# Optimization experiments

Measured on AMD Instinct MI355X. Metric: run time of the kernel, lower is better.

Reference implementation:

```python
import jax, jax.numpy as jnp
import numpy as np

SEQ_LEN, INPUT_DIM, HIDDEN_DIM, OUTPUT_DIM = 1024, 128, 256, 128
BATCH = 256


def setup_inputs() -> dict:
    key = jax.random.key(0)
    ks = jax.random.split(key, 12)
    s_x = 1.0 / np.sqrt(INPUT_DIM)
    s_h = 1.0 / np.sqrt(HIDDEN_DIM)
    def lin(k, fan_in, shape, scale):
        return jax.random.uniform(k, shape, jnp.float32, -scale, scale)
    inp = {"x": jax.random.normal(ks[0], (BATCH, SEQ_LEN, INPUT_DIM), jnp.float32)}
    names = ["g", "i", "f", "o"]
    for j, n in enumerate(names):
        inp[f"W{n}x"] = lin(ks[1 + 2 * j], INPUT_DIM, (HIDDEN_DIM, INPUT_DIM), s_x)
        inp[f"b{n}x"] = lin(jax.random.fold_in(ks[1 + 2 * j], 1), INPUT_DIM, (HIDDEN_DIM,), s_x)
        inp[f"W{n}h"] = lin(ks[2 + 2 * j], HIDDEN_DIM, (HIDDEN_DIM, HIDDEN_DIM), s_h)
    inp["Wp"] = lin(ks[9], HIDDEN_DIM, (OUTPUT_DIM, HIDDEN_DIM), s_h)
    inp["bp"] = lin(ks[10], HIDDEN_DIM, (OUTPUT_DIM,), s_h)
    return inp


def reference(x, Wgx, bgx, Wgh, Wix, bix, Wih, Wfx, bfx, Wfh, Wox, box, Woh, Wp, bp):
    B = x.shape[0]
    H = Wgh.shape[0]
    # Precompute all input projections in one batched GEMM per gate: (B,T,H)
    gx = jnp.einsum('bti,hi->bth', x, Wgx) + bgx
    ix = jnp.einsum('bti,hi->bth', x, Wix) + bix
    fx = jnp.einsum('bti,hi->bth', x, Wfx) + bfx
    ox = jnp.einsum('bti,hi->bth', x, Wox) + box
    xs = jnp.stack([gx, ix, fx, ox], axis=0).transpose(2, 0, 1, 3)  # (T,4,B,H)

    def step(carry, x_t):
        h, c = carry
        gx_t, ix_t, fx_t, ox_t = x_t[0], x_t[1], x_t[2], x_t[3]
        g = jnp.tanh(gx_t + h @ Wgh.T)
        i = jax.nn.sigmoid(ix_t + h @ Wih.T)
        f = jax.nn.sigmoid(fx_t + h @ Wfh.T)
        o = jax.nn.sigmoid(ox_t + h @ Woh.T)
        c = g * i + c * f
        h = jnp.tanh(c) * o
        return (h, c), None

    h0 = jnp.zeros((B, H), x.dtype)
    c0 = jnp.zeros((B, H), x.dtype)
    (h_T, _), _ = jax.lax.scan(step, (h0, c0), xs)
    return h_T @ Wp.T + bp
```

## Files before the change

### kernel.cpp

```cpp
#include <hip/hip_runtime.h>
#include <hip/hip_fp16.h>

#define TSEQ 1024
#define NBATCH 256
#define HD 256
#define ID 128
#define ODIM 128

typedef _Float16 f16;
typedef _Float16 f16x8 __attribute__((ext_vector_type(8)));
typedef float f32x4 __attribute__((ext_vector_type(4)));

__global__ void pack_weights(
    const float* __restrict__ Wgh, const float* __restrict__ Wih,
    const float* __restrict__ Wfh, const float* __restrict__ Woh,
    const float* __restrict__ Wgx, const float* __restrict__ Wix,
    const float* __restrict__ Wfx, const float* __restrict__ Wox,
    const float* __restrict__ bgx, const float* __restrict__ bix,
    const float* __restrict__ bfx, const float* __restrict__ box,
    f16* __restrict__ Whcat, f16* __restrict__ Wxcat, float* __restrict__ bcat)
{
    const int np = blockIdx.x;
    const int g  = (np >> 6) & 3;
    const int j  = np >> 8;
    const int uu = np & 63;
    const int u  = j * 64 + uu;
    const float* Wh = (g == 0) ? Wgh : (g == 1) ? Wih : (g == 2) ? Wfh : Woh;
    const float* Wx = (g == 0) ? Wgx : (g == 1) ? Wix : (g == 2) ? Wfx : Wox;
    const float* bx = (g == 0) ? bgx : (g == 1) ? bix : (g == 2) ? bfx : box;
    const int k = threadIdx.x;
    Whcat[np * 256 + k] = (f16)Wh[u * 256 + k];
    if (k < ID) Wxcat[np * ID + k] = (f16)Wx[u * ID + k];
    if (k == 0) bcat[np] = bx[u];
}

__global__ __launch_bounds__(256, 1) void lstm_rec(
    const float* __restrict__ x,
    const f16* __restrict__ Whcat,
    const f16* __restrict__ Wxcat,
    const float* __restrict__ bcat,
    f16* __restrict__ hbuf,
    float* __restrict__ hT,
    int* __restrict__ flags)
{
    const int tid  = threadIdx.x;
    const int lane = tid & 63;
    const int w    = tid >> 6;
    const int q    = lane >> 4;
    const int n    = lane & 15;
    const int bid  = blockIdx.x;
    const int grp  = bid >> 2;
    const int j    = bid & 3;
    const int b0   = grp * 16;

    f16x8 wh[4][8];
    f16x8 wx[4][4];
    float bias[4];
#pragma unroll
    for (int g = 0; g < 4; ++g) {
        const int row = j * 256 + g * 64 + w * 16 + n;
        bias[g] = bcat[row];
#pragma unroll
        for (int kk = 0; kk < 8; ++kk)
            wh[g][kk] = *(const f16x8*)&Whcat[row * 256 + kk * 32 + q * 8];
#pragma unroll
        for (int k4 = 0; k4 < 4; ++k4)
            wx[g][k4] = *(const f16x8*)&Wxcat[row * ID + k4 * 32 + q * 8];
    }

    float c[4] = {0.f, 0.f, 0.f, 0.f};
    const int uglob    = j * 64 + w * 16 + n;
    const int myslot   = (grp * 16 + j * 4 + w) * 64;
    const int pollslot = (grp * 16 + tid) * 64;

    const float* xrow = &x[(size_t)(b0 + n) * TSEQ * ID];
    float4 xr[8];
#pragma unroll
    for (int k4 = 0; k4 < 4; ++k4) {
        xr[k4 * 2]     = *(const float4*)&xrow[k4 * 32 + q * 8];
        xr[k4 * 2 + 1] = *(const float4*)&xrow[k4 * 32 + q * 8 + 4];
    }

    for (int t = 0; t < TSEQ; ++t) {
        f16x8 xa[4];
#pragma unroll
        for (int k4 = 0; k4 < 4; ++k4) {
            const float* f0 = (const float*)&xr[k4 * 2];
            const float* f1 = (const float*)&xr[k4 * 2 + 1];
#pragma unroll
            for (int e = 0; e < 4; ++e) {
                xa[k4][e]     = (f16)f0[e];
                xa[k4][4 + e] = (f16)f1[e];
            }
        }
        if (t + 1 < TSEQ) {
            const float* xp = &xrow[(size_t)(t + 1) * ID];
#pragma unroll
            for (int k4 = 0; k4 < 4; ++k4) {
                xr[k4 * 2]     = *(const float4*)&xp[k4 * 32 + q * 8];
                xr[k4 * 2 + 1] = *(const float4*)&xp[k4 * 32 + q * 8 + 4];
            }
        }

        f32x4 acc[4];
#pragma unroll
        for (int g = 0; g < 4; ++g) {
            f32x4 av = {bias[g], bias[g], bias[g], bias[g]};
            acc[g] = av;
        }
#pragma unroll
        for (int k4 = 0; k4 < 4; ++k4)
#pragma unroll
            for (int g = 0; g < 4; ++g)
                acc[g] = __builtin_amdgcn_mfma_f32_16x16x32_f16(xa[k4], wx[g][k4], acc[g], 0, 0, 0);

        if (t > 0) {
            if (tid < 16) {
                while (__hip_atomic_load(&flags[pollslot], __ATOMIC_RELAXED,
                                         __HIP_MEMORY_SCOPE_AGENT) < t)
                    __builtin_amdgcn_s_sleep(1);
            }
            __syncthreads();
            const unsigned long long* hp = (const unsigned long long*)
                &hbuf[(size_t)(((t - 1) & 1) * NBATCH + b0 + n) * HD];
            f16x8 ha[8];
#pragma unroll
            for (int kk = 0; kk < 8; ++kk) {
                union { unsigned long long u[2]; f16x8 v; } hu;
                hu.u[0] = __hip_atomic_load(hp + kk * 8 + q * 2,     __ATOMIC_RELAXED,
                                            __HIP_MEMORY_SCOPE_AGENT);
                hu.u[1] = __hip_atomic_load(hp + kk * 8 + q * 2 + 1, __ATOMIC_RELAXED,
                                            __HIP_MEMORY_SCOPE_AGENT);
                ha[kk] = hu.v;
            }
#pragma unroll
            for (int kk = 0; kk < 8; ++kk)
#pragma unroll
                for (int g = 0; g < 4; ++g)
                    acc[g] = __builtin_amdgcn_mfma_f32_16x16x32_f16(ha[kk], wh[g][kk], acc[g], 0, 0, 0);
        }

#pragma unroll
        for (int r = 0; r < 4; ++r) {
            const float gp_ = acc[0][r], ip_ = acc[1][r], fp_ = acc[2][r], op_ = acc[3][r];
            const float gg = 1.f - 2.f / (1.f + __expf(2.f * gp_));
            const float ii = 1.f / (1.f + __expf(-ip_));
            const float ff = 1.f / (1.f + __expf(-fp_));
            const float oo = 1.f / (1.f + __expf(-op_));
            c[r] = gg * ii + c[r] * ff;
            const float hh = (1.f - 2.f / (1.f + __expf(2.f * c[r]))) * oo;
            const int b = b0 + q * 4 + r;
            if (t < TSEQ - 1) {
                union { _Float16 f; unsigned short s; } cv;
                cv.f = (_Float16)hh;
                __hip_atomic_store((unsigned short*)&hbuf[(size_t)((t & 1) * NBATCH + b) * HD + uglob],
                                   cv.s, __ATOMIC_RELAXED, __HIP_MEMORY_SCOPE_AGENT);
            } else {
                hT[(size_t)b * HD + uglob] = hh;
            }
        }

        if (t < TSEQ - 1) {
            __atomic_signal_fence(__ATOMIC_SEQ_CST);
            __builtin_amdgcn_s_waitcnt(0x0F70);
            __atomic_signal_fence(__ATOMIC_SEQ_CST);
            if (lane == 0)
                __hip_atomic_store(&flags[myslot], t + 1, __ATOMIC_RELAXED,
                                   __HIP_MEMORY_SCOPE_AGENT);
        }
    }
}

__global__ void out_proj(const float* __restrict__ hT, const float* __restrict__ Wp,
                         const float* __restrict__ bp, float* __restrict__ out)
{
    const int b = blockIdx.x;
    const int o = threadIdx.x;
    __shared__ float hrow[HD];
    for (int u = threadIdx.x; u < HD; u += ODIM) hrow[u] = hT[b * HD + u];
    __syncthreads();
    float s = bp[o];
    const float* wr = &Wp[o * HD];
#pragma unroll 8
    for (int u = 0; u < HD; ++u) s += hrow[u] * wr[u];
    out[b * ODIM + o] = s;
}

extern "C" void kernel_launch(void* const* d_in, const int* in_sizes, int n_in,
                              void* d_out, int out_size, void* d_ws, size_t ws_size,
                              hipStream_t stream) {
    const float* x   = (const float*)d_in[0];
    const float* Wgx = (const float*)d_in[1];
    const float* bgx = (const float*)d_in[2];
    const float* Wgh = (const float*)d_in[3];
    const float* Wix = (const float*)d_in[4];
    const float* bix = (const float*)d_in[5];
    const float* Wih = (const float*)d_in[6];
    const float* Wfx = (const float*)d_in[7];
    const float* bfx = (const float*)d_in[8];
    const float* Wfh = (const float*)d_in[9];
    const float* Wox = (const float*)d_in[10];
    const float* box = (const float*)d_in[11];
    const float* Woh = (const float*)d_in[12];
    const float* Wp  = (const float*)d_in[13];
    const float* bp  = (const float*)d_in[14];
    float* out = (float*)d_out;

    char* ws = (char*)d_ws;
    f16*   Whcat = (f16*)(ws);
    f16*   Wxcat = (f16*)(ws + 524288);
    float* bcat  = (float*)(ws + 786432);
    f16*   hbuf  = (f16*)(ws + 790528);
    float* hT    = (float*)(ws + 1052672);
    int*   flags = (int*)(ws + 1314816);

    hipMemsetAsync(flags, 0, 256 * 64 * sizeof(int), stream);
    pack_weights<<<1024, 256, 0, stream>>>(Wgh, Wih, Wfh, Woh,
                                           Wgx, Wix, Wfx, Wox,
                                           bgx, bix, bfx, box,
                                           Whcat, Wxcat, bcat);
    lstm_rec<<<64, 256, 0, stream>>>(x, Whcat, Wxcat, bcat, hbuf, hT, flags);
    out_proj<<<NBATCH, ODIM, 0, stream>>>(hT, Wp, bp, out);
}
```

Baseline: 5.152 ms.

## Replace flag barriers with tagged hidden-state words and interleave two batch tiles

Each hidden value is now stored as a 32-bit word whose upper half carries the timestep, so consumers spin directly on the data instead of polling a separate flag after a waitcnt and a block barrier. Each block now handles two 16-row batch tiles, and the phases for the two tiles alternate. This lets one tile's recurrent loads and waits overlap with the other tile's compute, and the grid shrinks from 64 to 32 blocks. The cost is twice the bytes per hidden value, a full-vector compare on every poll, and fewer CUs in use.

```diff
diff --git a/kernel.cpp b/kernel.cpp
--- a/kernel.cpp
+++ b/kernel.cpp
@@ -6,10 +6,14 @@
 #define HD 256
 #define ID 128
 #define ODIM 128
+#define NGRP 8
+#define TILES 2
 
 typedef _Float16 f16;
 typedef _Float16 f16x8 __attribute__((ext_vector_type(8)));
 typedef float f32x4 __attribute__((ext_vector_type(4)));
+typedef unsigned int u32;
+typedef unsigned long long u64;
 
 __global__ void pack_weights(
     const float* __restrict__ Wgh, const float* __restrict__ Wih,
@@ -34,14 +38,37 @@
     if (k == 0) bcat[np] = bx[u];
 }
 
+
+__device__ __forceinline__ void load_xrow(const float* xp, int q, float4 (&xr)[8])
+{
+#pragma unroll
+    for (int k4 = 0; k4 < 4; ++k4) {
+        xr[k4 * 2]     = *(const float4*)&xp[k4 * 32 + q * 8];
+        xr[k4 * 2 + 1] = *(const float4*)&xp[k4 * 32 + q * 8 + 4];
+    }
+}
+
+__device__ __forceinline__ void conv_xa(const float4 (&xr)[8], f16x8 (&xa)[4])
+{
+#pragma unroll
+    for (int k4 = 0; k4 < 4; ++k4) {
+        const float* f0 = (const float*)&xr[k4 * 2];
+        const float* f1 = (const float*)&xr[k4 * 2 + 1];
+#pragma unroll
+        for (int e = 0; e < 4; ++e) {
+            xa[k4][e]     = (f16)f0[e];
+            xa[k4][4 + e] = (f16)f1[e];
+        }
+    }
+}
+
 __global__ __launch_bounds__(256, 1) void lstm_rec(
     const float* __restrict__ x,
     const f16* __restrict__ Whcat,
     const f16* __restrict__ Wxcat,
     const float* __restrict__ bcat,
-    f16* __restrict__ hbuf,
-    float* __restrict__ hT,
-    int* __restrict__ flags)
+    u32* __restrict__ hbt,
+    float* __restrict__ hT)
 {
     const int tid  = threadIdx.x;
     const int lane = tid & 63;
@@ -51,7 +78,6 @@
     const int bid  = blockIdx.x;
     const int grp  = bid >> 2;
     const int j    = bid & 3;
-    const int b0   = grp * 16;
 
     f16x8 wh[4][8];
     f16x8 wx[4][4];
@@ -68,78 +94,112 @@
             wx[g][k4] = *(const f16x8*)&Wxcat[row * ID + k4 * 32 + q * 8];
     }
 
-    float c[4] = {0.f, 0.f, 0.f, 0.f};
-    const int uglob    = j * 64 + w * 16 + n;
-    const int myslot   = (grp * 16 + j * 4 + w) * 64;
-    const int pollslot = (grp * 16 + tid) * 64;
-
-    const float* xrow = &x[(size_t)(b0 + n) * TSEQ * ID];
-    float4 xr[8];
-#pragma unroll
-    for (int k4 = 0; k4 < 4; ++k4) {
-        xr[k4 * 2]     = *(const float4*)&xrow[k4 * 32 + q * 8];
-        xr[k4 * 2 + 1] = *(const float4*)&xrow[k4 * 32 + q * 8 + 4];
-    }
-
-    for (int t = 0; t < TSEQ; ++t) {
+    const int uglob = j * 64 + w * 16 + n;
+    u32* gbase = hbt + (size_t)grp * (TILES * 2 * 16 * HD);
+    const float* xrow0 = &x[(size_t)(grp * 32 + n) * TSEQ * ID];
+    const float* xrow1 = &x[(size_t)(grp * 32 + 16 + n) * TSEQ * ID];
+
+    float4 xr0[8], xr1[8];
+    load_xrow(xrow0, q, xr0);
+    load_xrow(xrow1, q, xr1);
+
+    float c0[4] = {0.f, 0.f, 0.f, 0.f};
+    float c1[4] = {0.f, 0.f, 0.f, 0.f};
+    u64 hv[32];
+
+    auto prologue = [&](int k, const float* xrow, float4 (&xr)[8], float (&c)[4]) {
         f16x8 xa[4];
-#pragma unroll
-        for (int k4 = 0; k4 < 4; ++k4) {
-            const float* f0 = (const float*)&xr[k4 * 2];
-            const float* f1 = (const float*)&xr[k4 * 2 + 1];
-#pragma unroll
-            for (int e = 0; e < 4; ++e) {
-                xa[k4][e]     = (f16)f0[e];
-                xa[k4][4 + e] = (f16)f1[e];
-            }
-        }
-        if (t + 1 < TSEQ) {
-            const float* xp = &xrow[(size_t)(t + 1) * ID];
-#pragma unroll
-            for (int k4 = 0; k4 < 4; ++k4) {
-                xr[k4 * 2]     = *(const float4*)&xp[k4 * 32 + q * 8];
-                xr[k4 * 2 + 1] = *(const float4*)&xp[k4 * 32 + q * 8 + 4];
-            }
-        }
-
+        conv_xa(xr, xa);
+        load_xrow(xrow + ID, q, xr);
         f32x4 acc[4];
 #pragma unroll
-        for (int g = 0; g < 4; ++g) {
-            f32x4 av = {bias[g], bias[g], bias[g], bias[g]};
-            acc[g] = av;
-        }
+        for (int g = 0; g < 4; ++g) { f32x4 a = {bias[g], bias[g], bias[g], bias[g]}; acc[g] = a; }
 #pragma unroll
         for (int k4 = 0; k4 < 4; ++k4)
 #pragma unroll
             for (int g = 0; g < 4; ++g)
                 acc[g] = __builtin_amdgcn_mfma_f32_16x16x32_f16(xa[k4], wx[g][k4], acc[g], 0, 0, 0);
-
-        if (t > 0) {
-            if (tid < 16) {
-                while (__hip_atomic_load(&flags[pollslot], __ATOMIC_RELAXED,
-                                         __HIP_MEMORY_SCOPE_AGENT) < t)
-                    __builtin_amdgcn_s_sleep(1);
+        u32* sp = gbase + (size_t)((k * 2 + 0) * 16 + q * 4) * HD + uglob;
+#pragma unroll
+        for (int r = 0; r < 4; ++r) {
+            const float gp_ = acc[0][r], ip_ = acc[1][r], op_ = acc[3][r];
+            const float gg = 1.f - 2.f / (1.f + __expf(2.f * gp_));
+            const float ii = 1.f / (1.f + __expf(-ip_));
+            const float oo = 1.f / (1.f + __expf(-op_));
+            c[r] = gg * ii;
+            const float hh = (1.f - 2.f / (1.f + __expf(2.f * c[r]))) * oo;
+            union { _Float16 f; unsigned short s; } cv;
+            cv.f = (_Float16)hh;
+            __hip_atomic_store(sp + r * HD, (u32)cv.s, __ATOMIC_RELAXED, __HIP_MEMORY_SCOPE_AGENT);
+        }
+    };
+    prologue(0, xrow0, xr0, c0);
+    prologue(1, xrow1, xr1, c1);
+
+    {
+        const u64* hp = (const u64*)(gbase + (size_t)(0 * 16 + n) * HD) + q * 4;
+#pragma unroll
+        for (int kk = 0; kk < 8; ++kk)
+#pragma unroll
+            for (int m = 0; m < 4; ++m)
+                hv[kk * 4 + m] = __hip_atomic_load(hp + kk * 16 + m, __ATOMIC_RELAXED,
+                                                   __HIP_MEMORY_SCOPE_AGENT);
+    }
+
+    auto phase = [&](int t, int k, const float* xrow, float4 (&xr)[8], float (&c)[4]) {
+        f16x8 xa[4];
+        conv_xa(xr, xa);
+        const int tt = (t + 1 < TSEQ) ? t + 1 : TSEQ - 1;
+        load_xrow(xrow + (size_t)tt * ID, q, xr);
+
+        f32x4 acc[4];
+#pragma unroll
+        for (int g = 0; g < 4; ++g) { f32x4 a = {bias[g], bias[g], bias[g], bias[g]}; acc[g] = a; }
+#pragma unroll
+        for (int k4 = 0; k4 < 4; ++k4)
+#pragma unroll
+            for (int g = 0; g < 4; ++g)
+                acc[g] = __builtin_amdgcn_mfma_f32_16x16x32_f16(xa[k4], wx[g][k4], acc[g], 0, 0, 0);
+
+        const int pp = (t - 1) & 1;
+        const u64* hp = (const u64*)(gbase + (size_t)((k * 2 + pp) * 16 + n) * HD) + q * 4;
+        const u64 pat = (u64)(t - 1) * 0x0001000000010000ULL;
+        for (;;) {
+            u64 diff = 0;
+#pragma unroll
+            for (int i = 0; i < 32; ++i) diff |= hv[i] ^ pat;
+            if ((diff & 0xFFFF0000FFFF0000ULL) == 0ULL) break;
+#pragma unroll
+            for (int kk = 0; kk < 8; ++kk)
+#pragma unroll
+                for (int m = 0; m < 4; ++m)
+                    hv[kk * 4 + m] = __hip_atomic_load(hp + kk * 16 + m, __ATOMIC_RELAXED,
+                                                       __HIP_MEMORY_SCOPE_AGENT);
+        }
+
+        const int kn = k ^ 1;
+        const int pn = (k == 0) ? pp : (t & 1);
+        const u64* hpn = (const u64*)(gbase + (size_t)((kn * 2 + pn) * 16 + n) * HD) + q * 4;
+#pragma unroll
+        for (int kk = 0; kk < 8; ++kk) {
+            union { unsigned short us[8]; f16x8 v; } hu;
+#pragma unroll
+            for (int e2 = 0; e2 < 4; ++e2) {
+                const u64 d = hv[kk * 4 + e2];
+                hu.us[e2 * 2]     = (unsigned short)(d & 0xFFFFULL);
+                hu.us[e2 * 2 + 1] = (unsigned short)(d >> 32);
             }
-            __syncthreads();
-            const unsigned long long* hp = (const unsigned long long*)
-                &hbuf[(size_t)(((t - 1) & 1) * NBATCH + b0 + n) * HD];
-            f16x8 ha[8];
-#pragma unroll
-            for (int kk = 0; kk < 8; ++kk) {
-                union { unsigned long long u[2]; f16x8 v; } hu;
-                hu.u[0] = __hip_atomic_load(hp + kk * 8 + q * 2,     __ATOMIC_RELAXED,
-                                            __HIP_MEMORY_SCOPE_AGENT);
-                hu.u[1] = __hip_atomic_load(hp + kk * 8 + q * 2 + 1, __ATOMIC_RELAXED,
-                                            __HIP_MEMORY_SCOPE_AGENT);
-                ha[kk] = hu.v;
-            }
-#pragma unroll
-            for (int kk = 0; kk < 8; ++kk)
-#pragma unroll
-                for (int g = 0; g < 4; ++g)
-                    acc[g] = __builtin_amdgcn_mfma_f32_16x16x32_f16(ha[kk], wh[g][kk], acc[g], 0, 0, 0);
-        }
-
+#pragma unroll
+            for (int g = 0; g < 4; ++g)
+                acc[g] = __builtin_amdgcn_mfma_f32_16x16x32_f16(hu.v, wh[g][kk], acc[g], 0, 0, 0);
+#pragma unroll
+            for (int m = 0; m < 4; ++m)
+                hv[kk * 4 + m] = __hip_atomic_load(hpn + kk * 16 + m, __ATOMIC_RELAXED,
+                                                   __HIP_MEMORY_SCOPE_AGENT);
+        }
+
+        const u32 taghi = (u32)t << 16;
+        u32* sp = gbase + (size_t)((k * 2 + (t & 1)) * 16 + q * 4) * HD + uglob;
 #pragma unroll
         for (int r = 0; r < 4; ++r) {
             const float gp_ = acc[0][r], ip_ = acc[1][r], fp_ = acc[2][r], op_ = acc[3][r];
@@ -149,25 +209,21 @@
             const float oo = 1.f / (1.f + __expf(-op_));
             c[r] = gg * ii + c[r] * ff;
             const float hh = (1.f - 2.f / (1.f + __expf(2.f * c[r]))) * oo;
-            const int b = b0 + q * 4 + r;
             if (t < TSEQ - 1) {
                 union { _Float16 f; unsigned short s; } cv;
                 cv.f = (_Float16)hh;
-                __hip_atomic_store((unsigned short*)&hbuf[(size_t)((t & 1) * NBATCH + b) * HD + uglob],
-                                   cv.s, __ATOMIC_RELAXED, __HIP_MEMORY_SCOPE_AGENT);
+                __hip_atomic_store(sp + r * HD, taghi | (u32)cv.s, __ATOMIC_RELAXED,
+                                   __HIP_MEMORY_SCOPE_AGENT);
             } else {
+                const int b = grp * 32 + k * 16 + q * 4 + r;
                 hT[(size_t)b * HD + uglob] = hh;
             }
         }
-
-        if (t < TSEQ - 1) {
-            __atomic_signal_fence(__ATOMIC_SEQ_CST);
-            __builtin_amdgcn_s_waitcnt(0x0F70);
-            __atomic_signal_fence(__ATOMIC_SEQ_CST);
-            if (lane == 0)
-                __hip_atomic_store(&flags[myslot], t + 1, __ATOMIC_RELAXED,
-                                   __HIP_MEMORY_SCOPE_AGENT);
-        }
+    };
+
+    for (int t = 1; t < TSEQ; ++t) {
+        phase(t, 0, xrow0, xr0, c0);
+        phase(t, 1, xrow1, xr1, c1);
     }
 }
 
@@ -210,15 +266,14 @@
     f16*   Whcat = (f16*)(ws);
     f16*   Wxcat = (f16*)(ws + 524288);
     float* bcat  = (float*)(ws + 786432);
-    f16*   hbuf  = (f16*)(ws + 790528);
-    float* hT    = (float*)(ws + 1052672);
-    int*   flags = (int*)(ws + 1314816);
-
-    hipMemsetAsync(flags, 0, 256 * 64 * sizeof(int), stream);
+    u32*   hbt   = (u32*)(ws + 790528);
+    float* hT    = (float*)(ws + 1314816);
+
+    hipMemsetAsync(hbt, 0xFF, 524288, stream);
     pack_weights<<<1024, 256, 0, stream>>>(Wgh, Wih, Wfh, Woh,
                                            Wgx, Wix, Wfx, Wox,
                                            bgx, bix, bfx, box,
                                            Whcat, Wxcat, bcat);
-    lstm_rec<<<64, 256, 0, stream>>>(x, Whcat, Wxcat, bcat, hbuf, hT, flags);
+    lstm_rec<<<32, 256, 0, stream>>>(x, Whcat, Wxcat, bcat, hbt, hT);
     out_proj<<<NBATCH, ODIM, 0, stream>>>(hT, Wp, bp, out);
 }
```

Result: slower. 14.42 ms (+179.9%).

## Precompute input projections via GEMM and use tagged h exchange instead of flags

Applied to the files above, without the earlier changes.

Moves the per-step input projection out of the recurrent loop into a separate batched MFMA GEMM that writes fp16 gate preactivations to a large workspace buffer. The recurrent kernel now reads these preactivations with prefetching. Hidden-state exchange embeds a step tag in the upper 16 bits of each 32-bit word, so consumers poll the data itself and the per-step flag write, waitcnt and barrier are gone. Blocks are mapped onto XCDs, and a startup probe checks that all peer blocks are co-resident before taking the fast path; otherwise they fall back to a slow path. This adds a large workspace requirement and gx memory traffic, and uses bounded spin loops that break after a fixed number of tries.

```diff
diff --git a/kernel.cpp b/kernel.cpp
--- a/kernel.cpp
+++ b/kernel.cpp
@@ -10,6 +10,25 @@
 typedef _Float16 f16;
 typedef _Float16 f16x8 __attribute__((ext_vector_type(8)));
 typedef float f32x4 __attribute__((ext_vector_type(4)));
+typedef unsigned int u32;
+typedef unsigned int u32x4 __attribute__((ext_vector_type(4)));
+typedef unsigned long long u64;
+
+#define WS_WHCAT 0
+#define WS_WXCAT 524288
+#define WS_BCAT  786432
+#define WS_BCATG 790528
+#define WS_WXG   794624
+#define WS_HBT   1056768
+#define WS_HT    1581056
+#define WS_COMM  1843200
+#define WS_FLAGS 1843712
+#define WS_HBUF  1909248
+#define WS_GX    2171392
+#define WS_NEED  (2171392ULL + 536870912ULL)
+
+#define VMCNT_SB(n) do { asm volatile("s_waitcnt vmcnt(" #n ")" ::: "memory"); \
+                         __builtin_amdgcn_sched_barrier(0); } while (0)
 
 __global__ void pack_weights(
     const float* __restrict__ Wgh, const float* __restrict__ Wih,
@@ -18,7 +37,8 @@
     const float* __restrict__ Wfx, const float* __restrict__ Wox,
     const float* __restrict__ bgx, const float* __restrict__ bix,
     const float* __restrict__ bfx, const float* __restrict__ box,
-    f16* __restrict__ Whcat, f16* __restrict__ Wxcat, float* __restrict__ bcat)
+    f16* __restrict__ Whcat, f16* __restrict__ Wxcat, float* __restrict__ bcat,
+    float* __restrict__ bcatg, f16* __restrict__ Wxg)
 {
     const int np = blockIdx.x;
     const int g  = (np >> 6) & 3;
@@ -30,18 +50,474 @@
     const float* bx = (g == 0) ? bgx : (g == 1) ? bix : (g == 2) ? bfx : box;
     const int k = threadIdx.x;
     Whcat[np * 256 + k] = (f16)Wh[u * 256 + k];
-    if (k < ID) Wxcat[np * ID + k] = (f16)Wx[u * ID + k];
-    if (k == 0) bcat[np] = bx[u];
+    if (k < ID) {
+        Wxcat[np * ID + k] = (f16)Wx[u * ID + k];
+        Wxg[(size_t)(u * 4 + g) * ID + k] = (f16)Wx[u * ID + k];
+    }
+    if (k == 0) { bcat[np] = bx[u]; bcatg[u * 4 + g] = bx[u]; }
+}
+
+__global__ __launch_bounds__(256, 1) void xproj_gemm(
+    const float* __restrict__ x, const f16* __restrict__ Wxg,
+    const float* __restrict__ bcatg, f16* __restrict__ gx)
+{
+    const int tid = threadIdx.x, lane = tid & 63, w = tid >> 6;
+    const int q = lane >> 4, n = lane & 15;
+    const size_t R0 = (size_t)blockIdx.x * 32;
+    const int ncb = w * 256;
+
+    f16x8 a[2][4];
+#pragma unroll
+    for (int mb = 0; mb < 2; ++mb)
+#pragma unroll
+        for (int ks = 0; ks < 4; ++ks) {
+            const float* xp = &x[(R0 + mb * 16 + n) * ID + ks * 32 + q * 8];
+            float4 lo = *(const float4*)xp;
+            float4 hi = *(const float4*)(xp + 4);
+            f16x8 v;
+#pragma unroll
+            for (int e = 0; e < 4; ++e) { v[e] = (f16)(&lo.x)[e]; v[4 + e] = (f16)(&hi.x)[e]; }
+            a[mb][ks] = v;
+        }
+
+    f32x4 acc[2][16];
+#pragma unroll
+    for (int nb = 0; nb < 16; ++nb) {
+        const float bv = bcatg[ncb + nb * 16 + n];
+        f32x4 iv = {bv, bv, bv, bv};
+        acc[0][nb] = iv; acc[1][nb] = iv;
+    }
+
+#pragma unroll 4
+    for (int nb = 0; nb < 16; ++nb) {
+        const f16* bp = &Wxg[(size_t)(ncb + nb * 16 + n) * ID + q * 8];
+        const f16x8 b0 = *(const f16x8*)(bp);
+        const f16x8 b1 = *(const f16x8*)(bp + 32);
+        const f16x8 b2 = *(const f16x8*)(bp + 64);
+        const f16x8 b3 = *(const f16x8*)(bp + 96);
+#pragma unroll
+        for (int mb = 0; mb < 2; ++mb) {
+            acc[mb][nb] = __builtin_amdgcn_mfma_f32_16x16x32_f16(a[mb][0], b0, acc[mb][nb], 0, 0, 0);
+            acc[mb][nb] = __builtin_amdgcn_mfma_f32_16x16x32_f16(a[mb][1], b1, acc[mb][nb], 0, 0, 0);
+            acc[mb][nb] = __builtin_amdgcn_mfma_f32_16x16x32_f16(a[mb][2], b2, acc[mb][nb], 0, 0, 0);
+            acc[mb][nb] = __builtin_amdgcn_mfma_f32_16x16x32_f16(a[mb][3], b3, acc[mb][nb], 0, 0, 0);
+        }
+    }
+
+#pragma unroll
+    for (int mb = 0; mb < 2; ++mb)
+#pragma unroll
+        for (int nb = 0; nb < 16; ++nb)
+#pragma unroll
+            for (int r = 0; r < 4; ++r)
+                gx[(R0 + mb * 16 + q * 4 + r) * 1024 + (ncb + nb * 16 + n)] =
+                    (f16)acc[mb][nb][r];
+}
+
+__device__ __forceinline__ void hv_issue8_fast(const u32* hp, u32x4 (&hv)[8])
+{
+    asm volatile(
+        "global_load_dwordx4 %0, %8, off sc0\n\t"
+        "global_load_dwordx4 %1, %8, off offset:16 sc0\n\t"
+        "global_load_dwordx4 %2, %8, off offset:128 sc0\n\t"
+        "global_load_dwordx4 %3, %8, off offset:144 sc0\n\t"
+        "global_load_dwordx4 %4, %8, off offset:256 sc0\n\t"
+        "global_load_dwordx4 %5, %8, off offset:272 sc0\n\t"
+        "global_load_dwordx4 %6, %8, off offset:384 sc0\n\t"
+        "global_load_dwordx4 %7, %8, off offset:400 sc0"
+        : "=&v"(hv[0]), "=&v"(hv[1]), "=&v"(hv[2]), "=&v"(hv[3]),
+          "=&v"(hv[4]), "=&v"(hv[5]), "=&v"(hv[6]), "=&v"(hv[7])
+        : "v"(hp) : "memory");
+}
+
+__device__ __forceinline__ void gx_issue(const f16* g0, const f16* g1,
+                                         const f16* g2, const f16* g3, u64 (&gd)[4])
+{
+    asm volatile(
+        "global_load_dwordx2 %0, %4, off\n\t"
+        "global_load_dwordx2 %1, %5, off\n\t"
+        "global_load_dwordx2 %2, %6, off\n\t"
+        "global_load_dwordx2 %3, %7, off"
+        : "=&v"(gd[0]), "=&v"(gd[1]), "=&v"(gd[2]), "=&v"(gd[3])
+        : "v"(g0), "v"(g1), "v"(g2), "v"(g3) : "memory");
+}
+
+__device__ __forceinline__ void h_store4_fast(u32* sp, u32 a, u32 b, u32 c, u32 d)
+{
+    asm volatile(
+        "global_store_dword %4, %0, off sc0\n\t"
+        "global_store_dword %4, %1, off offset:1024 sc0\n\t"
+        "global_store_dword %4, %2, off offset:2048 sc0\n\t"
+        "global_store_dword %4, %3, off offset:3072 sc0"
+        :: "v"(a), "v"(b), "v"(c), "v"(d), "v"(sp) : "memory");
+}
+
+__device__ __forceinline__ bool tags_ok(const u32x4 (&hv)[8], u32 taghi)
+{
+    u32 d = 0;
+#pragma unroll
+    for (int i = 0; i < 8; ++i)
+        d |= (hv[i][0] ^ taghi) | (hv[i][1] ^ taghi) | (hv[i][2] ^ taghi) | (hv[i][3] ^ taghi);
+    return (d & 0xFFFF0000u) == 0u;
+}
+
+__device__ __forceinline__ f16x8 mk_frag(u32x4 a, u32x4 b)
+{
+    union { unsigned short us[8]; f16x8 v; } u;
+#pragma unroll
+    for (int e = 0; e < 4; ++e) {
+        u.us[e]     = (unsigned short)(a[e] & 0xFFFFu);
+        u.us[4 + e] = (unsigned short)(b[e] & 0xFFFFu);
+    }
+    return u.v;
+}
+
+__device__ __forceinline__ void gx_unpack(const u64 (&gd)[4], f32x4 (&acc)[4])
+{
+    union { u64 u; _Float16 h[4]; } t0, t1, t2, t3;
+    t0.u = gd[0]; t1.u = gd[1]; t2.u = gd[2]; t3.u = gd[3];
+#pragma unroll
+    for (int g = 0; g < 4; ++g) {
+        f32x4 a;
+        a[0] = (float)t0.h[g]; a[1] = (float)t1.h[g];
+        a[2] = (float)t2.h[g]; a[3] = (float)t3.h[g];
+        acc[g] = a;
+    }
+}
+
+__device__ void lstm_fast(const f16* __restrict__ Whcat, const f16* __restrict__ gx,
+                          u32* __restrict__ hbt, float* __restrict__ hT,
+                          int tid, int grp, int j)
+{
+    const int lane = tid & 63, w = tid >> 6, q = lane >> 4, n = lane & 15;
+    const int b0 = grp * 16;
+    const int uglob = j * 64 + w * 16 + n;
+
+    f16x8 wh[4][8];
+#pragma unroll
+    for (int g = 0; g < 4; ++g) {
+        const int row = j * 256 + g * 64 + w * 16 + n;
+#pragma unroll
+        for (int kk = 0; kk < 8; ++kk)
+            wh[g][kk] = *(const f16x8*)&Whcat[row * 256 + kk * 32 + q * 8];
+    }
+
+    u32* gbase = hbt + (size_t)grp * (2 * 16 * HD);
+    const u32* hp0 = gbase + (size_t)(0 * 16 + n) * HD + q * 8;
+    const u32* hp1 = gbase + (size_t)(1 * 16 + n) * HD + q * 8;
+
+    const f16* gp0 = gx + (size_t)(b0 + q * 4 + 0) * TSEQ * 1024 + (size_t)uglob * 4;
+    const f16* gp1 = gx + (size_t)(b0 + q * 4 + 1) * TSEQ * 1024 + (size_t)uglob * 4;
+    const f16* gp2 = gx + (size_t)(b0 + q * 4 + 2) * TSEQ * 1024 + (size_t)uglob * 4;
+    const f16* gp3 = gx + (size_t)(b0 + q * 4 + 3) * TSEQ * 1024 + (size_t)uglob * 4;
+
+    float c[4] = {0.f, 0.f, 0.f, 0.f};
+    u64 gxA[4], gxB[4];
+
+    gx_issue(gp0, gp1, gp2, gp3, gxA);
+    gp0 += 1024; gp1 += 1024; gp2 += 1024; gp3 += 1024;
+    VMCNT_SB(0);
+    {
+        f32x4 acc[4];
+        gx_unpack(gxA, acc);
+        gx_issue(gp0, gp1, gp2, gp3, gxB);
+        gp0 += 1024; gp1 += 1024; gp2 += 1024; gp3 += 1024;
+        u32 hwv[4];
+#pragma unroll
+        for (int r = 0; r < 4; ++r) {
+            const float gp_ = acc[0][r], ip_ = acc[1][r], fp_ = acc[2][r], op_ = acc[3][r];
+            const float gg = 1.f - 2.f / (1.f + __expf(2.f * gp_));
+            const float ii = 1.f / (1.f + __expf(-ip_));
+            const float ff = 1.f / (1.f + __expf(-fp_));
+            const float oo = 1.f / (1.f + __expf(-op_));
+            c[r] = gg * ii + c[r] * ff;
+            const float hh = (1.f - 2.f / (1.f + __expf(2.f * c[r]))) * oo;
+            union { _Float16 f; unsigned short s; } cv; cv.f = (_Float16)hh;
+            hwv[r] = (u32)cv.s;
+        }
+        u32* sp = gbase + (size_t)(0 * 16 + q * 4) * HD + uglob;
+        h_store4_fast(sp, hwv[0], hwv[1], hwv[2], hwv[3]);
+    }
+
+    auto stepMid = [&](int t, u64 (&gU)[4], u64 (&gI)[4]) {
+        const u32* hp = ((t - 1) & 1) ? hp1 : hp0;
+        const u32 taghiP = (u32)(t - 1) << 16;
+        u32x4 hv[8];
+        hv_issue8_fast(hp, hv);
+        gx_issue(gp0, gp1, gp2, gp3, gI);
+        gp0 += 1024; gp1 += 1024; gp2 += 1024; gp3 += 1024;
+        VMCNT_SB(12);
+        f32x4 acc[4];
+        gx_unpack(gU, acc);
+        VMCNT_SB(4);
+        int tries = 0;
+        while (!tags_ok(hv, taghiP)) {
+            if (++tries > 16384) break;
+            hv_issue8_fast(hp, hv);
+            VMCNT_SB(4);
+        }
+        const f16x8 ha0 = mk_frag(hv[0], hv[1]);
+        const f16x8 ha1 = mk_frag(hv[2], hv[3]);
+        const f16x8 ha2 = mk_frag(hv[4], hv[5]);
+        const f16x8 ha3 = mk_frag(hv[6], hv[7]);
+        u32x4 hv2[8];
+        hv_issue8_fast(hp + 128, hv2);
+#pragma unroll
+        for (int g = 0; g < 4; ++g) {
+            acc[g] = __builtin_amdgcn_mfma_f32_16x16x32_f16(ha0, wh[g][0], acc[g], 0, 0, 0);
+            acc[g] = __builtin_amdgcn_mfma_f32_16x16x32_f16(ha1, wh[g][1], acc[g], 0, 0, 0);
+            acc[g] = __builtin_amdgcn_mfma_f32_16x16x32_f16(ha2, wh[g][2], acc[g], 0, 0, 0);
+            acc[g] = __builtin_amdgcn_mfma_f32_16x16x32_f16(ha3, wh[g][3], acc[g], 0, 0, 0);
+        }
+        VMCNT_SB(4);
+        tries = 0;
+        while (!tags_ok(hv2, taghiP)) {
+            if (++tries > 16384) break;
+            hv_issue8_fast(hp + 128, hv2);
+            VMCNT_SB(4);
+        }
+        const f16x8 hb0 = mk_frag(hv2[0], hv2[1]);
+        const f16x8 hb1 = mk_frag(hv2[2], hv2[3]);
+        const f16x8 hb2 = mk_frag(hv2[4], hv2[5]);
+        const f16x8 hb3 = mk_frag(hv2[6], hv2[7]);
+#pragma unroll
+        for (int g = 0; g < 4; ++g) {
+            acc[g] = __builtin_amdgcn_mfma_f32_16x16x32_f16(hb0, wh[g][4], acc[g], 0, 0, 0);
+            acc[g] = __builtin_amdgcn_mfma_f32_16x16x32_f16(hb1, wh[g][5], acc[g], 0, 0, 0);
+            acc[g] = __builtin_amdgcn_mfma_f32_16x16x32_f16(hb2, wh[g][6], acc[g], 0, 0, 0);
+            acc[g] = __builtin_amdgcn_mfma_f32_16x16x32_f16(hb3, wh[g][7], acc[g], 0, 0, 0);
+        }
+        const u32 taghi = (u32)t << 16;
+        u32 hwv[4];
+#pragma unroll
+        for (int r = 0; r < 4; ++r) {
+            const float gp_ = acc[0][r], ip_ = acc[1][r], fp_ = acc[2][r], op_ = acc[3][r];
+            const float gg = 1.f - 2.f / (1.f + __expf(2.f * gp_));
+            const float ii = 1.f / (1.f + __expf(-ip_));
+            const float ff = 1.f / (1.f + __expf(-fp_));
+            const float oo = 1.f / (1.f + __expf(-op_));
+            c[r] = gg * ii + c[r] * ff;
+            const float hh = (1.f - 2.f / (1.f + __expf(2.f * c[r]))) * oo;
+            union { _Float16 f; unsigned short s; } cv; cv.f = (_Float16)hh;
+            hwv[r] = taghi | (u32)cv.s;
+        }
+        u32* sp = gbase + (size_t)(((t & 1) * 16 + q * 4)) * HD + uglob;
+        h_store4_fast(sp, hwv[0], hwv[1], hwv[2], hwv[3]);
+    };
+
+    for (int t = 1; t <= 1021; t += 2) {
+        stepMid(t,     gxB, gxA);
+        stepMid(t + 1, gxA, gxB);
+    }
+
+    {
+        const int t = 1023;
+        const u32* hp = hp0;
+        const u32 taghiP = (u32)(t - 1) << 16;
+        u32x4 hv[8];
+        hv_issue8_fast(hp, hv);
+        VMCNT_SB(8);
+        f32x4 acc[4];
+        gx_unpack(gxB, acc);
+        VMCNT_SB(0);
+        int tries = 0;
+        while (!tags_ok(hv, taghiP)) {
+            if (++tries > 16384) break;
+            hv_issue8_fast(hp, hv);
+            VMCNT_SB(0);
+        }
+        const f16x8 ha0 = mk_frag(hv[0], hv[1]);
+        const f16x8 ha1 = mk_frag(hv[2], hv[3]);
+        const f16x8 ha2 = mk_frag(hv[4], hv[5]);
+        const f16x8 ha3 = mk_frag(hv[6], hv[7]);
+        u32x4 hv2[8];
+        hv_issue8_fast(hp + 128, hv2);
+#pragma unroll
+        for (int g = 0; g < 4; ++g) {
+            acc[g] = __builtin_amdgcn_mfma_f32_16x16x32_f16(ha0, wh[g][0], acc[g], 0, 0, 0);
+            acc[g] = __builtin_amdgcn_mfma_f32_16x16x32_f16(ha1, wh[g][1], acc[g], 0, 0, 0);
+            acc[g] = __builtin_amdgcn_mfma_f32_16x16x32_f16(ha2, wh[g][2], acc[g], 0, 0, 0);
+            acc[g] = __builtin_amdgcn_mfma_f32_16x16x32_f16(ha3, wh[g][3], acc[g], 0, 0, 0);
+        }
+        VMCNT_SB(0);
+        tries = 0;
+        while (!tags_ok(hv2, taghiP)) {
+            if (++tries > 16384) break;
+            hv_issue8_fast(hp + 128, hv2);
+            VMCNT_SB(0);
+        }
+        const f16x8 hb0 = mk_frag(hv2[0], hv2[1]);
+        const f16x8 hb1 = mk_frag(hv2[2], hv2[3]);
+        const f16x8 hb2 = mk_frag(hv2[4], hv2[5]);
+        const f16x8 hb3 = mk_frag(hv2[6], hv2[7]);
+#pragma unroll
+        for (int g = 0; g < 4; ++g) {
+            acc[g] = __builtin_amdgcn_mfma_f32_16x16x32_f16(hb0, wh[g][4], acc[g], 0, 0, 0);
+            acc[g] = __builtin_amdgcn_mfma_f32_16x16x32_f16(hb1, wh[g][5], acc[g], 0, 0, 0);
+            acc[g] = __builtin_amdgcn_mfma_f32_16x16x32_f16(hb2, wh[g][6], acc[g], 0, 0, 0);
+            acc[g] = __builtin_amdgcn_mfma_f32_16x16x32_f16(hb3, wh[g][7], acc[g], 0, 0, 0);
+        }
+#pragma unroll
+        for (int r = 0; r < 4; ++r) {
+            const float gp_ = acc[0][r], ip_ = acc[1][r], fp_ = acc[2][r], op_ = acc[3][r];
+            const float gg = 1.f - 2.f / (1.f + __expf(2.f * gp_));
+            const float ii = 1.f / (1.f + __expf(-ip_));
+            const float ff = 1.f / (1.f + __expf(-fp_));
+            const float oo = 1.f / (1.f + __expf(-op_));
+            c[r] = gg * ii + c[r] * ff;
+            const float hh = (1.f - 2.f / (1.f + __expf(2.f * c[r]))) * oo;
+            hT[(size_t)(b0 + q * 4 + r) * HD + uglob] = hh;
+        }
+    }
+}
+
+__device__ void lstm_slow(const f16* __restrict__ Whcat, const f16* __restrict__ gx,
+                          u32* __restrict__ hbt, float* __restrict__ hT,
+                          int tid, int grp, int j)
+{
+    const int lane = tid & 63, w = tid >> 6, q = lane >> 4, n = lane & 15;
+    const int b0 = grp * 16;
+    const int uglob = j * 64 + w * 16 + n;
+
+    f16x8 wh[4][8];
+#pragma unroll
+    for (int g = 0; g < 4; ++g) {
+        const int row = j * 256 + g * 64 + w * 16 + n;
+#pragma unroll
+        for (int kk = 0; kk < 8; ++kk)
+            wh[g][kk] = *(const f16x8*)&Whcat[row * 256 + kk * 32 + q * 8];
+    }
+
+    u32* gbase = hbt + (size_t)grp * (2 * 16 * HD);
+    const f16* gpr[1]; (void)gpr;
+    const f16* gpb0 = gx + (size_t)(b0 + q * 4 + 0) * TSEQ * 1024 + (size_t)uglob * 4;
+    const f16* gpb1 = gx + (size_t)(b0 + q * 4 + 1) * TSEQ * 1024 + (size_t)uglob * 4;
+    const f16* gpb2 = gx + (size_t)(b0 + q * 4 + 2) * TSEQ * 1024 + (size_t)uglob * 4;
+    const f16* gpb3 = gx + (size_t)(b0 + q * 4 + 3) * TSEQ * 1024 + (size_t)uglob * 4;
+    float c[4] = {0.f, 0.f, 0.f, 0.f};
+
+    for (int t = 0; t < TSEQ; ++t) {
+        u64 gd[4];
+        gd[0] = *(const u64*)gpb0; gd[1] = *(const u64*)gpb1;
+        gd[2] = *(const u64*)gpb2; gd[3] = *(const u64*)gpb3;
+        gpb0 += 1024; gpb1 += 1024; gpb2 += 1024; gpb3 += 1024;
+        f32x4 acc[4];
+        gx_unpack(gd, acc);
+
+        if (t > 0) {
+            const int pp = (t - 1) & 1;
+            const u32* hp = gbase + (size_t)(pp * 16 + n) * HD + q * 8;
+            const u32 taghiP = (u32)(t - 1) << 16;
+            u32 hvw[64];
+            int tries = 0;
+            for (;;) {
+#pragma unroll
+                for (int kk = 0; kk < 8; ++kk)
+#pragma unroll
+                    for (int e = 0; e < 8; ++e)
+                        hvw[kk * 8 + e] = __hip_atomic_load(hp + kk * 32 + e,
+                                            __ATOMIC_RELAXED, __HIP_MEMORY_SCOPE_AGENT);
+                u32 d = 0;
+#pragma unroll
+                for (int i = 0; i < 64; ++i) d |= hvw[i] ^ taghiP;
+                if ((d & 0xFFFF0000u) == 0u) break;
+                if (++tries > 16384) break;
+                __builtin_amdgcn_s_sleep(2);
+            }
+#pragma unroll
+            for (int kk = 0; kk < 8; ++kk) {
+                union { unsigned short us[8]; f16x8 v; } hu;
+#pragma unroll
+                for (int e = 0; e < 8; ++e)
+                    hu.us[e] = (unsigned short)(hvw[kk * 8 + e] & 0xFFFFu);
+#pragma unroll
+                for (int g = 0; g < 4; ++g)
+                    acc[g] = __builtin_amdgcn_mfma_f32_16x16x32_f16(hu.v, wh[g][kk], acc[g], 0, 0, 0);
+            }
+        }
+
+        const u32 taghi = (u32)t << 16;
+        u32* sp = gbase + (size_t)(((t & 1) * 16 + q * 4)) * HD + uglob;
+#pragma unroll
+        for (int r = 0; r < 4; ++r) {
+            const float gp_ = acc[0][r], ip_ = acc[1][r], fp_ = acc[2][r], op_ = acc[3][r];
+            const float gg = 1.f - 2.f / (1.f + __expf(2.f * gp_));
+            const float ii = 1.f / (1.f + __expf(-ip_));
+            const float ff = 1.f / (1.f + __expf(-fp_));
+            const float oo = 1.f / (1.f + __expf(-op_));
+            c[r] = gg * ii + c[r] * ff;
+            const float hh = (1.f - 2.f / (1.f + __expf(2.f * c[r]))) * oo;
+            if (t < TSEQ - 1) {
+                union { _Float16 f; unsigned short s; } cv; cv.f = (_Float16)hh;
+                __hip_atomic_store(sp + r * HD, taghi | (u32)cv.s,
+                                   __ATOMIC_RELAXED, __HIP_MEMORY_SCOPE_AGENT);
+            } else {
+                hT[(size_t)(b0 + q * 4 + r) * HD + uglob] = hh;
+            }
+        }
+    }
 }
 
 __global__ __launch_bounds__(256, 1) void lstm_rec(
+    const f16* __restrict__ Whcat, const f16* __restrict__ gx,
+    u32* __restrict__ hbt, float* __restrict__ hT, u32* __restrict__ comm)
+{
+    const int tid  = threadIdx.x;
+    const int bid  = blockIdx.x;
+    const int xcd  = bid & 7;
+    const int j    = (bid >> 3) & 3;
+    const int half = bid >> 5;
+    const int grp  = xcd * 2 + half;
+
+    __shared__ int s_fast;
+    if (tid == 0) {
+        u32* probe = comm;
+        u32* flg   = comm + 64;
+        const u32 salt = 0xA5C30000u;
+        {
+            const u32 v = salt | (u32)bid;
+            asm volatile("global_store_dword %0, %1, off sc0\n\ts_waitcnt vmcnt(0)"
+                         :: "v"(&probe[bid]), "v"(v) : "memory");
+        }
+        const int need = 0xF ^ (1 << j);
+        int seen = 0;
+        for (int it = 0; it < 2048 && seen != need; ++it) {
+#pragma unroll
+            for (int m = 0; m < 4; ++m) {
+                if (m == j || (seen & (1 << m))) continue;
+                const int pb = half * 32 + m * 8 + xcd;
+                u32 v;
+                asm volatile("global_load_dword %0, %1, off sc0\n\ts_waitcnt vmcnt(0)"
+                             : "=&v"(v) : "v"(&probe[pb]) : "memory");
+                if (v == (salt | (u32)pb)) seen |= (1 << m);
+            }
+        }
+        const u32 ok = (seen == need) ? 2u : 1u;
+        __hip_atomic_store(&flg[bid], ok, __ATOMIC_RELAXED, __HIP_MEMORY_SCOPE_AGENT);
+        int allok = (ok == 2u);
+        for (int m = 0; m < 4; ++m) {
+            if (m == j) continue;
+            const int pb = half * 32 + m * 8 + xcd;
+            u32 v = 0; int it2 = 0;
+            do {
+                v = __hip_atomic_load(&flg[pb], __ATOMIC_RELAXED, __HIP_MEMORY_SCOPE_AGENT);
+            } while (v == 0u && ++it2 < (1 << 20));
+            allok &= (v == 2u);
+        }
+        s_fast = allok;
+    }
+    __syncthreads();
+
+    if (s_fast) lstm_fast(Whcat, gx, hbt, hT, tid, grp, j);
+    else        lstm_slow(Whcat, gx, hbt, hT, tid, grp, j);
+}
+
+__global__ __launch_bounds__(256, 1) void lstm_rec_fb(
     const float* __restrict__ x,
     const f16* __restrict__ Whcat,
     const f16* __restrict__ Wxcat,
     const float* __restrict__ bcat,
-    f16* __restrict__ hbuf,
-    float* __restrict__ hT,
-    int* __restrict__ flags)
+    f16* __restrict__ hbuf, float* __restrict__ hT, int* __restrict__ flags)
 {
     const int tid  = threadIdx.x;
     const int lane = tid & 63;
@@ -104,10 +580,7 @@
 
         f32x4 acc[4];
 #pragma unroll
-        for (int g = 0; g < 4; ++g) {
-            f32x4 av = {bias[g], bias[g], bias[g], bias[g]};
-            acc[g] = av;
-        }
+        for (int g = 0; g < 4; ++g) { f32x4 av = {bias[g], bias[g], bias[g], bias[g]}; acc[g] = av; }
 #pragma unroll
         for (int k4 = 0; k4 < 4; ++k4)
 #pragma unroll
@@ -207,18 +680,32 @@
     float* out = (float*)d_out;
 
     char* ws = (char*)d_ws;
-    f16*   Whcat = (f16*)(ws);
-    f16*   Wxcat = (f16*)(ws + 524288);
-    float* bcat  = (float*)(ws + 786432);
-    f16*   hbuf  = (f16*)(ws + 790528);
-    float* hT    = (float*)(ws + 1052672);
-    int*   flags = (int*)(ws + 1314816);
-
-    hipMemsetAsync(flags, 0, 256 * 64 * sizeof(int), stream);
+    f16*   Whcat = (f16*)(ws + WS_WHCAT);
+    f16*   Wxcat = (f16*)(ws + WS_WXCAT);
+    float* bcat  = (float*)(ws + WS_BCAT);
+    float* bcatg = (float*)(ws + WS_BCATG);
+    f16*   Wxg   = (f16*)(ws + WS_WXG);
+    u32*   hbt   = (u32*)(ws + WS_HBT);
+    float* hT    = (float*)(ws + WS_HT);
+    u32*   comm  = (u32*)(ws + WS_COMM);
+    int*   flags = (int*)(ws + WS_FLAGS);
+    f16*   hbuf  = (f16*)(ws + WS_HBUF);
+    f16*   gxbuf = (f16*)(ws + WS_GX);
+
+    hipMemsetAsync(hbt, 0xFF, 524288, stream);
+    hipMemsetAsync(comm, 0, 512, stream);
+    hipMemsetAsync(flags, 0, 65536, stream);
+
     pack_weights<<<1024, 256, 0, stream>>>(Wgh, Wih, Wfh, Woh,
                                            Wgx, Wix, Wfx, Wox,
                                            bgx, bix, bfx, box,
-                                           Whcat, Wxcat, bcat);
-    lstm_rec<<<64, 256, 0, stream>>>(x, Whcat, Wxcat, bcat, hbuf, hT, flags);
+                                           Whcat, Wxcat, bcat, bcatg, Wxg);
+
+    if (ws_size >= WS_NEED) {
+        xproj_gemm<<<8192, 256, 0, stream>>>(x, Wxg, bcatg, gxbuf);
+        lstm_rec<<<64, 256, 0, stream>>>(Whcat, gxbuf, hbt, hT, comm);
+    } else {
+        lstm_rec_fb<<<64, 256, 0, stream>>>(x, Whcat, Wxcat, bcat, hbuf, hT, flags);
+    }
     out_proj<<<NBATCH, ODIM, 0, stream>>>(hT, Wp, bp, out);
 }
```

After: 5.189 ms. Within noise of the previous version (+0.7%).
